# Performance work log

Hardware: AMD Instinct MI355X
Metric: run time of the kernel (lower is better)

## Reference

```python
import jax, jax.numpy as jnp
import numpy as np

EPS_ATTN = 1e-6
LN_EPS = 1e-5

def _layernorm(x, g, b):
    mu = jnp.mean(x, axis=-1, keepdims=True)
    var = jnp.var(x, axis=-1, keepdims=True)
    return (x - mu) * jax.lax.rsqrt(var + LN_EPS) * g + b

def _phi(x):
    return jax.nn.elu(x) + 1.0

def setup_inputs() -> dict:
    key = jax.random.key(0)
    ks = jax.random.split(key, 8)
    B, T, D, H = 2, 4096, 128, 128  # D = token_dim = d+1, H = hidden_dim
    s = 0.02
    return {
        "tokens": jax.random.normal(ks[0], (B, T, D), dtype=jnp.float32),
        "Wq": jax.random.normal(ks[1], (D, H), dtype=jnp.float32) * s,
        "Wk": jax.random.normal(ks[2], (D, H), dtype=jnp.float32) * s,
        "Wv": jax.random.normal(ks[3], (D, D), dtype=jnp.float32) * s,
        "Wg": jax.random.normal(ks[4], (D, D), dtype=jnp.float32) * s,
        "bg": jnp.zeros((D,), dtype=jnp.float32),
        "Wo": jax.random.normal(ks[5], (D, D), dtype=jnp.float32) * s,
        "g1": jnp.ones((D,), dtype=jnp.float32),
        "b1": jnp.zeros((D,), dtype=jnp.float32),
        "g2": jnp.ones((D,), dtype=jnp.float32),
        "b2": jnp.zeros((D,), dtype=jnp.float32),
    }

def reference(tokens, Wq, Wk, Wv, Wg, bg, Wo, g1, b1, g2, b2):
    x = _layernorm(tokens, g1, b1)                 # (b,t,m)
    Q = x @ Wq                                     # (b,t,h)
    K = x @ Wk                                     # (b,t,h)
    V = x @ Wv                                     # (b,t,m)
    G = jax.nn.sigmoid(x @ Wg + bg)                # (b,t,m)
    Vg = V * G
    Qp = _phi(Q)
    Kp = _phi(K)
    # causal linear attention via cumulative outer products
    kv = jnp.einsum('bth,btm->bthm', Kp, Vg)       # (b,t,h,m)
    S_kv = jnp.cumsum(kv, axis=1)
    S_k = jnp.cumsum(Kp, axis=1)
    numerator = jnp.einsum('bth,bthm->btm', Qp, S_kv)
    denom = jnp.maximum(jnp.einsum('bth,bth->bt', Qp, S_k), EPS_ATTN)
    attn_out = numerator / denom[..., None]
    out = tokens + (attn_out @ Wo) * 0.1
    return _layernorm(out, g2, b2)
```

## Files before the change

kernel.cpp:

```cpp
#include <hip/hip_runtime.h>
#include <math.h>

#define D_ 128
#define NTOK 8192
#define CHUNK 64
#define NCB 64
#define NCH 128
#define LN_EPS 1e-5f
#define EPS_ATTN 1e-6f

typedef __attribute__((ext_vector_type(8))) short bf16x8;
typedef __attribute__((ext_vector_type(4))) short bf16x4;
typedef __attribute__((ext_vector_type(2))) short bf16x2;
typedef __attribute__((ext_vector_type(4))) float f32x4;

__device__ inline short f2bf(float f) {
  unsigned u = __builtin_bit_cast(unsigned, f);
  u += 0x7fffu + ((u >> 16) & 1u);
  return (short)(u >> 16);
}
__device__ inline float bf2f(short s) {
  unsigned u = ((unsigned)(unsigned short)s) << 16;
  return __builtin_bit_cast(float, u);
}
__device__ inline float phi_(float x) { return x > 0.f ? x + 1.f : __expf(x); }

__global__ __launch_bounds__(256) void k_prep(const float* __restrict__ tokens,
    const float* __restrict__ Wq, const float* __restrict__ Wk,
    const float* __restrict__ Wv, const float* __restrict__ Wg,
    const float* __restrict__ Wo,
    const float* __restrict__ g1, const float* __restrict__ b1,
    short* __restrict__ WT, short* __restrict__ xln) {
  const int tid = threadIdx.x, bid = blockIdx.x;
  __shared__ float lds[64][132];
  if (bid < 10) {
    const int mat = bid >> 1, half = bid & 1;
    const float* W = mat==0?Wq: mat==1?Wk: mat==2?Wv: mat==3?Wg:Wo;
    short* o = WT + mat*D_*D_;
    #pragma unroll
    for (int it = 0; it < 8; ++it) {
      const int f = it*1024 + tid*4;
      const int kk = f >> 7, n = f & 127;
      const float4 v = *(const float4*)&W[(half*64 + kk)*D_ + n];
      lds[kk][n] = v.x; lds[kk][n+1] = v.y; lds[kk][n+2] = v.z; lds[kk][n+3] = v.w;
    }
    __syncthreads();
    #pragma unroll
    for (int it = 0; it < 8; ++it) {
      const int f = it*1024 + tid*4;
      const int n = f >> 6, kl = f & 63;
      bf16x4 ov;
      ov.x = f2bf(lds[kl][n]);   ov.y = f2bf(lds[kl+1][n]);
      ov.z = f2bf(lds[kl+2][n]); ov.w = f2bf(lds[kl+3][n]);
      *(bf16x4*)&o[n*D_ + half*64 + kl] = ov;
    }
    return;
  }
  const int m0 = (bid - 10) * 32;
  const int w = tid >> 6, l = tid & 63;
  const float2 gg = *(const float2*)&g1[l*2];
  const float2 bb = *(const float2*)&b1[l*2];
  float2 tv[8];
  #pragma unroll
  for (int it = 0; it < 8; ++it)
    tv[it] = *(const float2*)&tokens[(m0 + w*8 + it)*D_ + l*2];
  #pragma unroll
  for (int it = 0; it < 8; ++it) {
    const float2 v = tv[it];
    float s = v.x + v.y, qq = v.x*v.x + v.y*v.y;
    #pragma unroll
    for (int off = 1; off < 64; off <<= 1) {
      s += __shfl_xor(s, off); qq += __shfl_xor(qq, off);
    }
    const float mean = s*(1.f/D_);
    const float r2 = rsqrtf(qq*(1.f/D_) - mean*mean + LN_EPS);
    bf16x2 o;
    o.x = f2bf((v.x-mean)*r2*gg.x + bb.x);
    o.y = f2bf((v.y-mean)*r2*gg.y + bb.y);
    *(bf16x2*)&xln[(m0 + w*8 + it)*D_ + l*2] = o;
  }
}

__global__ __launch_bounds__(256) void k_qkvg(const short* __restrict__ xln,
    const short* __restrict__ WT, const float* __restrict__ bgp,
    short* __restrict__ Qp, short* __restrict__ Kp, short* __restrict__ KpT,
    short* __restrict__ VgT) {
  const int tid = threadIdx.x, bid = blockIdx.x;
  const int w = tid >> 6, l = tid & 63;
  const int i = l & 15, q = l >> 4;
  __shared__ short xs[32][136];
  __shared__ short wsd[128][136];

  auto stageW = [&](const short* __restrict__ Wb) {
    for (int v = tid; v < 2048; v += 256) {
      const int n = v >> 4, c8 = (v & 15)*8;
      *(bf16x8*)&wsd[n][c8] = *(const bf16x8*)&Wb[n*D_ + c8];
    }
  };
  auto stageX = [&](int m0) {
    for (int u = tid; u < 512; u += 256) {
      const int t = u >> 4, c8 = (u & 15)*8;
      *(bf16x8*)&xs[t][c8] = *(const bf16x8*)&xln[(m0 + t)*D_ + c8];
    }
  };
  auto gemm = [&](f32x4 (*acc)[2]) {
    #pragma unroll
    for (int kk = 0; kk < 4; ++kk) {
      bf16x8 a[2], bfr[2];
      #pragma unroll
      for (int mt = 0; mt < 2; ++mt) a[mt] = *(const bf16x8*)&xs[mt*16+i][kk*32+q*8];
      #pragma unroll
      for (int nt = 0; nt < 2; ++nt) bfr[nt] = *(const bf16x8*)&wsd[w*32+nt*16+i][kk*32+q*8];
      #pragma unroll
      for (int mt = 0; mt < 2; ++mt)
        #pragma unroll
        for (int nt = 0; nt < 2; ++nt)
          acc[mt][nt] = __builtin_amdgcn_mfma_f32_16x16x32_bf16(a[mt], bfr[nt], acc[mt][nt], 0, 0, 0);
    }
  };

  if (bid < 256) {
    const int m0 = bid * 32;
    stageX(m0);
    stageW(WT + 2*D_*D_);
    __syncthreads();
    f32x4 acc[2][2], accg[2][2];
    #pragma unroll
    for (int mt = 0; mt < 2; ++mt)
      #pragma unroll
      for (int nt = 0; nt < 2; ++nt) acc[mt][nt] = (f32x4){0.f,0.f,0.f,0.f};
    gemm(acc);
    __syncthreads();
    stageW(WT + 3*D_*D_);
    __syncthreads();
    #pragma unroll
    for (int mt = 0; mt < 2; ++mt)
      #pragma unroll
      for (int nt = 0; nt < 2; ++nt) accg[mt][nt] = (f32x4){0.f,0.f,0.f,0.f};
    gemm(accg);
    #pragma unroll
    for (int mt = 0; mt < 2; ++mt)
      #pragma unroll
      for (int nt = 0; nt < 2; ++nt) {
        const int h = w*32 + nt*16 + i;
        const int t0 = m0 + mt*16 + 4*q;
        const float bgd = bgp[h];
        bf16x4 o;
        #pragma unroll
        for (int r = 0; r < 4; ++r) {
          const float gv = 1.f/(1.f + __expf(-(accg[mt][nt][r] + bgd)));
          o[r] = f2bf(acc[mt][nt][r] * gv);
        }
        *(bf16x4*)&VgT[h*NTOK + t0] = o;
      }
  } else if (bid < 384) {
    stageW(WT);
    for (int uu = 0; uu < 2; ++uu) {
      const int m0 = ((bid - 256)*2 + uu) * 32;
      __syncthreads();
      stageX(m0);
      __syncthreads();
      f32x4 acc[2][2];
      #pragma unroll
      for (int mt = 0; mt < 2; ++mt)
        #pragma unroll
        for (int nt = 0; nt < 2; ++nt) acc[mt][nt] = (f32x4){0.f,0.f,0.f,0.f};
      gemm(acc);
      #pragma unroll
      for (int mt = 0; mt < 2; ++mt)
        #pragma unroll
        for (int nt = 0; nt < 2; ++nt) {
          const int h = w*32 + nt*16 + i;
          #pragma unroll
          for (int r = 0; r < 4; ++r)
            Qp[(m0 + mt*16 + 4*q + r)*D_ + h] = f2bf(phi_(acc[mt][nt][r]));
        }
    }
  } else {
    stageW(WT + D_*D_);
    for (int uu = 0; uu < 2; ++uu) {
      const int m0 = ((bid - 384)*2 + uu) * 32;
      __syncthreads();
      stageX(m0);
      __syncthreads();
      f32x4 acc[2][2];
      #pragma unroll
      for (int mt = 0; mt < 2; ++mt)
        #pragma unroll
        for (int nt = 0; nt < 2; ++nt) acc[mt][nt] = (f32x4){0.f,0.f,0.f,0.f};
      gemm(acc);
      #pragma unroll
      for (int mt = 0; mt < 2; ++mt)
        #pragma unroll
        for (int nt = 0; nt < 2; ++nt) {
          const int h = w*32 + nt*16 + i;
          const int t0 = m0 + mt*16 + 4*q;
          bf16x4 o;
          #pragma unroll
          for (int r = 0; r < 4; ++r) {
            const short bv = f2bf(phi_(acc[mt][nt][r]));
            Kp[(t0+r)*D_ + h] = bv;
            o[r] = bv;
          }
          *(bf16x4*)&KpT[h*NTOK + t0] = o;
        }
    }
  }
}

__global__ __launch_bounds__(256) void k_cs(const short* __restrict__ KpT,
    const short* __restrict__ VgT, const short* __restrict__ Qp,
    const short* __restrict__ Kp,
    float* __restrict__ KVT, float* __restrict__ Ksum,
    short* __restrict__ A, float* __restrict__ rowsum) {
  const int tid = threadIdx.x, bid = blockIdx.x;
  const int w = tid >> 6, l = tid & 63;
  const int i = l & 15, q = l >> 4;
  __shared__ __align__(16) char smem[34816];

  auto chunkkv = [&](int v) {
    const int c = v & 127, hh = (v >> 7) & 1, dh = v >> 8;
    const int tb = c*CHUNK;
    short (*vgl)[72] = (short(*)[72])smem;
    short (*kpl)[72] = (short(*)[72])(smem + 9216);
    float (*ksp)[5]  = (float(*)[5])(smem + 18432);
    for (int u = tid; u < 512; u += 256) {
      const int dd = u >> 3, c8 = (u & 7)*8;
      *(bf16x8*)&vgl[dd][c8] = *(const bf16x8*)&VgT[(dh*64+dd)*NTOK + tb + c8];
      *(bf16x8*)&kpl[dd][c8] = *(const bf16x8*)&KpT[(hh*64+dd)*NTOK + tb + c8];
    }
    __syncthreads();
    f32x4 acc[4];
    #pragma unroll
    for (int nt = 0; nt < 4; ++nt) acc[nt] = (f32x4){0.f,0.f,0.f,0.f};
    #pragma unroll
    for (int kk = 0; kk < 2; ++kk) {
      bf16x8 a = *(const bf16x8*)&vgl[w*16+i][kk*32+q*8];
      #pragma unroll
      for (int nt = 0; nt < 4; ++nt) {
        bf16x8 bb = *(const bf16x8*)&kpl[nt*16+i][kk*32+q*8];
        acc[nt] = __builtin_amdgcn_mfma_f32_16x16x32_bf16(a, bb, acc[nt], 0, 0, 0);
      }
    }
    float* KVc = KVT + (size_t)c*16384;
    #pragma unroll
    for (int nt = 0; nt < 4; ++nt)
      #pragma unroll
      for (int r = 0; r < 4; ++r) {
        const int d = dh*64 + w*16 + 4*q + r;
        const int h = hh*64 + nt*16 + i;
        KVc[d*D_ + h] = acc[nt][r];
      }
    if (dh == 0) {
      const int hq = tid >> 2, part = tid & 3;
      float s = 0.f;
      #pragma unroll
      for (int t = 0; t < 16; ++t) s += bf2f(kpl[hq][part*16 + t]);
      ksp[hq][part] = s;
      __syncthreads();
      if (tid < 64)
        Ksum[c*D_ + hh*64 + tid] = ksp[tid][0]+ksp[tid][1]+ksp[tid][2]+ksp[tid][3];
    }
  };

  auto scores = [&](int c) {
    const int tb = c*CHUNK;
    short (*qpl)[136] = (short(*)[136])smem;
    short (*kpl)[136] = (short(*)[136])(smem + 17408);
    for (int u = tid; u < 1024; u += 256) {
      const int t = u >> 4, c8 = (u & 15)*8;
      *(bf16x8*)&qpl[t][c8] = *(const bf16x8*)&Qp[(tb+t)*D_ + c8];
      *(bf16x8*)&kpl[t][c8] = *(const bf16x8*)&Kp[(tb+t)*D_ + c8];
    }
    __syncthreads();
    f32x4 acc[4];
    #pragma unroll
    for (int nt = 0; nt < 4; ++nt) acc[nt] = (f32x4){0.f,0.f,0.f,0.f};
    #pragma unroll
    for (int kk = 0; kk < 4; ++kk) {
      bf16x8 a = *(const bf16x8*)&qpl[w*16+i][kk*32+q*8];
      #pragma unroll
      for (int nt = 0; nt < 4; ++nt) {
        if (nt <= w) {
          bf16x8 bb = *(const bf16x8*)&kpl[nt*16+i][kk*32+q*8];
          acc[nt] = __builtin_amdgcn_mfma_f32_16x16x32_bf16(a, bb, acc[nt], 0, 0, 0);
        }
      }
    }
    short* Ac = A + c*4096;
    float rs[4] = {0.f,0.f,0.f,0.f};
    #pragma unroll
    for (int nt = 0; nt < 4; ++nt) {
      #pragma unroll
      for (int r = 0; r < 4; ++r) {
        const int t = w*16 + 4*q + r;
        const int s = nt*16 + i;
        const float v = (nt <= w && s <= t) ? acc[nt][r] : 0.f;
        rs[r] += v;
        Ac[t*64 + s] = f2bf(v);
      }
    }
    #pragma unroll
    for (int r = 0; r < 4; ++r) {
      #pragma unroll
      for (int off = 1; off < 16; off <<= 1) rs[r] += __shfl_xor(rs[r], off);
    }
    if (i == 0) {
      #pragma unroll
      for (int r = 0; r < 4; ++r) rowsum[c*64 + w*16 + 4*q + r] = rs[r];
    }
  };

  if (bid < 128) {
    scores(bid);
    __syncthreads();
    chunkkv(384 + bid);
  } else {
    chunkkv(bid - 128);
  }
}

__global__ __launch_bounds__(256) void k_scan(const float* __restrict__ KVT,
    short* __restrict__ KVTb, float* __restrict__ Ksum) {
  const int tid = threadIdx.x;
  if (blockIdx.x < 128) {
    const int b = blockIdx.x >> 6;
    const int e = (blockIdx.x & 63)*256 + tid;
    const size_t base = (size_t)b*NCB*16384 + e;
    float run = 0.f;
    #pragma unroll 8
    for (int c = 0; c < NCB; ++c) {
      const float v = KVT[base + (size_t)c*16384];
      KVTb[base + (size_t)c*16384] = f2bf(run);
      run += v;
    }
    return;
  }
  const int b = tid >> 7, h = tid & 127;
  float run = 0.f;
  #pragma unroll 8
  for (int c = 0; c < NCB; ++c) {
    const int idx = (b*NCB + c)*128 + h;
    const float v = Ksum[idx];
    Ksum[idx] = run;
    run += v;
  }
}

__global__ __launch_bounds__(256) void k_attnout(const short* __restrict__ Aintra,
    const short* __restrict__ Qp, const short* __restrict__ VgT,
    const short* __restrict__ KVTb, const float* __restrict__ Ksum,
    const float* __restrict__ rowsum, short* __restrict__ attn) {
  const int bid = blockIdx.x, tid = threadIdx.x;
  const int c = bid & 127, dq = bid >> 7;
  const int tb = c*CHUNK;
  __shared__ short at[64][200], bt[32][200];
  __shared__ float ksl[128], dpart[64][4], denl[64];
  const short* Ac = Aintra + c*4096;
  #pragma unroll
  for (int u = tid; u < 512; u += 256) {
    const int t = u >> 3, c8 = (u & 7)*8;
    *(bf16x8*)&at[t][c8] = *(const bf16x8*)&Ac[t*64 + c8];
  }
  #pragma unroll
  for (int u = tid; u < 1024; u += 256) {
    const int t = u >> 4, c8 = (u & 15)*8;
    *(bf16x8*)&at[t][64 + c8] = *(const bf16x8*)&Qp[(tb+t)*D_ + c8];
  }
  for (int u = tid; u < 256; u += 256) {
    const int dd = u >> 3, c8 = (u & 7)*8;
    *(bf16x8*)&bt[dd][c8] = *(const bf16x8*)&VgT[(dq*32+dd)*NTOK + tb + c8];
  }
  #pragma unroll
  for (int u = tid; u < 512; u += 256) {
    const int dd = u >> 4, c8 = (u & 15)*8;
    *(bf16x8*)&bt[dd][64 + c8] = *(const bf16x8*)&KVTb[(size_t)c*16384 + (dq*32+dd)*D_ + c8];
  }
  if (tid < 128) ksl[tid] = Ksum[c*128 + tid];
  __syncthreads();
  {
    const int t = tid >> 2, part = tid & 3;
    float dot = 0.f;
    #pragma unroll
    for (int h = 0; h < 32; ++h) dot += bf2f(at[t][64 + part*32 + h]) * ksl[part*32 + h];
    dpart[t][part] = dot;
  }
  __syncthreads();
  if (tid < 64)
    denl[tid] = fmaxf(rowsum[c*64 + tid] + dpart[tid][0]+dpart[tid][1]+dpart[tid][2]+dpart[tid][3], EPS_ATTN);
  __syncthreads();
  const int w = tid >> 6, l = tid & 63, i = l & 15, q = l >> 4;
  f32x4 acc[2];
  #pragma unroll
  for (int nt = 0; nt < 2; ++nt) acc[nt] = (f32x4){0.f,0.f,0.f,0.f};
  #pragma unroll
  for (int kk = 0; kk < 6; ++kk) {
    bf16x8 a = *(const bf16x8*)&at[w*16+i][kk*32+q*8];
    #pragma unroll
    for (int nt = 0; nt < 2; ++nt) {
      bf16x8 bb = *(const bf16x8*)&bt[nt*16+i][kk*32+q*8];
      acc[nt] = __builtin_amdgcn_mfma_f32_16x16x32_bf16(a, bb, acc[nt], 0, 0, 0);
    }
  }
  #pragma unroll
  for (int r = 0; r < 4; ++r) {
    const int t = w*16 + 4*q + r;
    const float inv = 1.f / denl[t];
    #pragma unroll
    for (int nt = 0; nt < 2; ++nt)
      attn[(size_t)(tb+t)*D_ + dq*32 + nt*16 + i] = f2bf(acc[nt][r] * inv);
  }
}

__global__ __launch_bounds__(256) void k_outln2(const short* __restrict__ attn,
    const short* __restrict__ WoT, const float* __restrict__ tokens,
    const float* __restrict__ g2, const float* __restrict__ b2,
    float* __restrict__ out) {
  const int m0 = blockIdx.x*32, tid = threadIdx.x;
  __shared__ short al[32][136], wl[128][136];
  __shared__ float tl[32][132];
  __shared__ float suml[32][4], ssql[32][4];
  __shared__ float meanl[32], rstdl[32];
  __shared__ float gl[128], bl2[128];
  for (int u = tid; u < 512; u += 256) {
    const int t = u >> 4, c8 = (u & 15)*8;
    *(bf16x8*)&al[t][c8] = *(const bf16x8*)&attn[(m0+t)*D_ + c8];
  }
  #pragma unroll
  for (int u = tid; u < 2048; u += 256) {
    const int n = u >> 4, c8 = (u & 15)*8;
    *(bf16x8*)&wl[n][c8] = *(const bf16x8*)&WoT[n*D_ + c8];
  }
  #pragma unroll
  for (int u = tid; u < 1024; u += 256) {
    const int t = u >> 5, c4 = (u & 31)*4;
    *(float4*)&tl[t][c4] = *(const float4*)&tokens[(m0+t)*D_ + c4];
  }
  if (tid < 128) { gl[tid] = g2[tid]; bl2[tid] = b2[tid]; }
  __syncthreads();
  const int w = tid >> 6, l = tid & 63, i = l & 15, q = l >> 4;
  f32x4 acc[2][2];
  #pragma unroll
  for (int mt = 0; mt < 2; ++mt)
    #pragma unroll
    for (int j = 0; j < 2; ++j) acc[mt][j] = (f32x4){0.f,0.f,0.f,0.f};
  #pragma unroll
  for (int kk = 0; kk < 4; ++kk) {
    bf16x8 a[2];
    #pragma unroll
    for (int mt = 0; mt < 2; ++mt) a[mt] = *(const bf16x8*)&al[mt*16+i][kk*32+q*8];
    #pragma unroll
    for (int j = 0; j < 2; ++j) {
      bf16x8 bb = *(const bf16x8*)&wl[(w*2+j)*16+i][kk*32+q*8];
      #pragma unroll
      for (int mt = 0; mt < 2; ++mt)
        acc[mt][j] = __builtin_amdgcn_mfma_f32_16x16x32_bf16(a[mt], bb, acc[mt][j], 0, 0, 0);
    }
  }
  float p[2][4][2];
  #pragma unroll
  for (int mt = 0; mt < 2; ++mt)
    #pragma unroll
    for (int r = 0; r < 4; ++r) {
      const int t = mt*16 + 4*q + r;
      float ps = 0.f, qs = 0.f;
      #pragma unroll
      for (int j = 0; j < 2; ++j) {
        const int col = w*32 + j*16 + i;
        const float v = tl[t][col] + 0.1f*acc[mt][j][r];
        p[mt][r][j] = v; ps += v; qs += v*v;
      }
      #pragma unroll
      for (int off = 1; off < 16; off <<= 1) {
        ps += __shfl_xor(ps, off); qs += __shfl_xor(qs, off);
      }
      if (i == 0) { suml[t][w] = ps; ssql[t][w] = qs; }
    }
  __syncthreads();
  if (tid < 32) {
    const float s = suml[tid][0]+suml[tid][1]+suml[tid][2]+suml[tid][3];
    const float qq = ssql[tid][0]+ssql[tid][1]+ssql[tid][2]+ssql[tid][3];
    const float mean = s*(1.f/D_);
    meanl[tid] = mean;
    rstdl[tid] = rsqrtf(qq*(1.f/D_) - mean*mean + LN_EPS);
  }
  __syncthreads();
  #pragma unroll
  for (int mt = 0; mt < 2; ++mt)
    #pragma unroll
    for (int r = 0; r < 4; ++r) {
      const int t = mt*16 + 4*q + r;
      const float mean = meanl[t], rr = rstdl[t];
      #pragma unroll
      for (int j = 0; j < 2; ++j) {
        const int col = w*32 + j*16 + i;
        out[(m0+t)*D_ + col] = (p[mt][r][j]-mean)*rr*gl[col] + bl2[col];
      }
    }
}

extern "C" void kernel_launch(void* const* d_in, const int* in_sizes, int n_in,
                              void* d_out, int out_size, void* d_ws, size_t ws_size,
                              hipStream_t stream) {
  const float* tokens = (const float*)d_in[0];
  const float* Wq = (const float*)d_in[1];
  const float* Wk = (const float*)d_in[2];
  const float* Wv = (const float*)d_in[3];
  const float* Wg = (const float*)d_in[4];
  const float* bg = (const float*)d_in[5];
  const float* Wo = (const float*)d_in[6];
  const float* g1 = (const float*)d_in[7];
  const float* b1 = (const float*)d_in[8];
  const float* g2 = (const float*)d_in[9];
  const float* b2 = (const float*)d_in[10];

  char* base = (char*)d_ws;
  short* Qp     = (short*)(base);
  short* Kp     = (short*)(base + (2u<<20));
  short* KpT    = (short*)(base + (4u<<20));
  short* VgT    = (short*)(base + (6u<<20));
  short* attn   = (short*)(base + (8u<<20));
  short* KVTb   = (short*)(base + (10u<<20));
  short* Aintra = (short*)(base + (14u<<20));
  short* WT     = (short*)(base + (15u<<20));
  float* rowsum = (float*)(base + (15u<<20) + (256u<<10));
  float* Ksum   = (float*)(base + (15u<<20) + (512u<<10));
  float* KVT    = (float*)(base + (16u<<20));
  short* xln    = (short*)(base + (24u<<20));

  short* WoT = WT + 4*D_*D_;

  k_prep<<<266, 256, 0, stream>>>(tokens, Wq, Wk, Wv, Wg, Wo, g1, b1, WT, xln);
  k_qkvg<<<512, 256, 0, stream>>>(xln, WT, bg, Qp, Kp, KpT, VgT);
  k_cs<<<512, 256, 0, stream>>>(KpT, VgT, Qp, Kp, KVT, Ksum, Aintra, rowsum);
  k_scan<<<129, 256, 0, stream>>>(KVT, KVTb, Ksum);
  k_attnout<<<512, 256, 0, stream>>>(Aintra, Qp, VgT, KVTb, Ksum, rowsum, attn);
  k_outln2<<<NTOK/32, 256, 0, stream>>>(attn, WoT, tokens, g2, b2, (float*)d_out);
}
```

Measured before the change: 112.6 us.

## Fuse LayerNorm and weight prep into QKVG, fuse attention output with Wo+LN2

Removes the separate prep kernel: each QKVG block now computes LayerNorm of its token rows directly into shared memory and transposes/converts the fp32 weights to bf16 while staging them. Attention output and the final Wo projection plus second LayerNorm are merged into one kernel. Each block handles 32 rows with all 128 output columns, and the normalized attention result stays in shared memory. This drops two launches and the xln/attn round trips through global memory. The cost is redundant weight conversion in every block, LayerNorm recomputed in Q and K blocks, and larger shared memory use with fewer blocks in the fused output kernel.

After: 112.8 us. No clear change (+0.1%).

```diff
diff --git a/kernel.cpp b/kernel.cpp
--- a/kernel.cpp
+++ b/kernel.cpp
@@ -25,64 +25,11 @@
 }
 __device__ inline float phi_(float x) { return x > 0.f ? x + 1.f : __expf(x); }
 
-__global__ __launch_bounds__(256) void k_prep(const float* __restrict__ tokens,
+__global__ __launch_bounds__(256) void k_qkvg(const float* __restrict__ tokens,
     const float* __restrict__ Wq, const float* __restrict__ Wk,
     const float* __restrict__ Wv, const float* __restrict__ Wg,
-    const float* __restrict__ Wo,
+    const float* __restrict__ bgp,
     const float* __restrict__ g1, const float* __restrict__ b1,
-    short* __restrict__ WT, short* __restrict__ xln) {
-  const int tid = threadIdx.x, bid = blockIdx.x;
-  __shared__ float lds[64][132];
-  if (bid < 10) {
-    const int mat = bid >> 1, half = bid & 1;
-    const float* W = mat==0?Wq: mat==1?Wk: mat==2?Wv: mat==3?Wg:Wo;
-    short* o = WT + mat*D_*D_;
-    #pragma unroll
-    for (int it = 0; it < 8; ++it) {
-      const int f = it*1024 + tid*4;
-      const int kk = f >> 7, n = f & 127;
-      const float4 v = *(const float4*)&W[(half*64 + kk)*D_ + n];
-      lds[kk][n] = v.x; lds[kk][n+1] = v.y; lds[kk][n+2] = v.z; lds[kk][n+3] = v.w;
-    }
-    __syncthreads();
-    #pragma unroll
-    for (int it = 0; it < 8; ++it) {
-      const int f = it*1024 + tid*4;
-      const int n = f >> 6, kl = f & 63;
-      bf16x4 ov;
-      ov.x = f2bf(lds[kl][n]);   ov.y = f2bf(lds[kl+1][n]);
-      ov.z = f2bf(lds[kl+2][n]); ov.w = f2bf(lds[kl+3][n]);
-      *(bf16x4*)&o[n*D_ + half*64 + kl] = ov;
-    }
-    return;
-  }
-  const int m0 = (bid - 10) * 32;
-  const int w = tid >> 6, l = tid & 63;
-  const float2 gg = *(const float2*)&g1[l*2];
-  const float2 bb = *(const float2*)&b1[l*2];
-  float2 tv[8];
-  #pragma unroll
-  for (int it = 0; it < 8; ++it)
-    tv[it] = *(const float2*)&tokens[(m0 + w*8 + it)*D_ + l*2];
-  #pragma unroll
-  for (int it = 0; it < 8; ++it) {
-    const float2 v = tv[it];
-    float s = v.x + v.y, qq = v.x*v.x + v.y*v.y;
-    #pragma unroll
-    for (int off = 1; off < 64; off <<= 1) {
-      s += __shfl_xor(s, off); qq += __shfl_xor(qq, off);
-    }
-    const float mean = s*(1.f/D_);
-    const float r2 = rsqrtf(qq*(1.f/D_) - mean*mean + LN_EPS);
-    bf16x2 o;
-    o.x = f2bf((v.x-mean)*r2*gg.x + bb.x);
-    o.y = f2bf((v.y-mean)*r2*gg.y + bb.y);
-    *(bf16x2*)&xln[(m0 + w*8 + it)*D_ + l*2] = o;
-  }
-}
-
-__global__ __launch_bounds__(256) void k_qkvg(const short* __restrict__ xln,
-    const short* __restrict__ WT, const float* __restrict__ bgp,
     short* __restrict__ Qp, short* __restrict__ Kp, short* __restrict__ KpT,
     short* __restrict__ VgT) {
   const int tid = threadIdx.x, bid = blockIdx.x;
@@ -91,16 +38,39 @@
   __shared__ short xs[32][136];
   __shared__ short wsd[128][136];
 
-  auto stageW = [&](const short* __restrict__ Wb) {
-    for (int v = tid; v < 2048; v += 256) {
-      const int n = v >> 4, c8 = (v & 15)*8;
-      *(bf16x8*)&wsd[n][c8] = *(const bf16x8*)&Wb[n*D_ + c8];
+  auto stageWT = [&](const float* __restrict__ Wf) {
+    #pragma unroll
+    for (int it = 0; it < 16; ++it) {
+      const int v = it*256 + tid;
+      const int k = v & 127, n4 = v >> 7;
+      const float4 x4 = *(const float4*)&Wf[k*D_ + n4*4];
+      wsd[n4*4+0][k] = f2bf(x4.x);
+      wsd[n4*4+1][k] = f2bf(x4.y);
+      wsd[n4*4+2][k] = f2bf(x4.z);
+      wsd[n4*4+3][k] = f2bf(x4.w);
     }
   };
-  auto stageX = [&](int m0) {
-    for (int u = tid; u < 512; u += 256) {
-      const int t = u >> 4, c8 = (u & 15)*8;
-      *(bf16x8*)&xs[t][c8] = *(const bf16x8*)&xln[(m0 + t)*D_ + c8];
+  auto doLN = [&](int m0) {
+    const float2 gg = *(const float2*)&g1[l*2];
+    const float2 bb = *(const float2*)&b1[l*2];
+    float2 tv[8];
+    #pragma unroll
+    for (int it = 0; it < 8; ++it)
+      tv[it] = *(const float2*)&tokens[(m0 + w*8 + it)*D_ + l*2];
+    #pragma unroll
+    for (int it = 0; it < 8; ++it) {
+      const float2 v = tv[it];
+      float s = v.x + v.y, qq = v.x*v.x + v.y*v.y;
+      #pragma unroll
+      for (int off = 1; off < 64; off <<= 1) {
+        s += __shfl_xor(s, off); qq += __shfl_xor(qq, off);
+      }
+      const float mean = s*(1.f/D_);
+      const float r2 = rsqrtf(qq*(1.f/D_) - mean*mean + LN_EPS);
+      bf16x2 o;
+      o.x = f2bf((v.x-mean)*r2*gg.x + bb.x);
+      o.y = f2bf((v.y-mean)*r2*gg.y + bb.y);
+      *(bf16x2*)&xs[w*8 + it][l*2] = o;
     }
   };
   auto gemm = [&](f32x4 (*acc)[2]) {
@@ -121,8 +91,8 @@
 
   if (bid < 256) {
     const int m0 = bid * 32;
-    stageX(m0);
-    stageW(WT + 2*D_*D_);
+    doLN(m0);
+    stageWT(Wv);
     __syncthreads();
     f32x4 acc[2][2], accg[2][2];
     #pragma unroll
@@ -131,7 +101,7 @@
       for (int nt = 0; nt < 2; ++nt) acc[mt][nt] = (f32x4){0.f,0.f,0.f,0.f};
     gemm(acc);
     __syncthreads();
-    stageW(WT + 3*D_*D_);
+    stageWT(Wg);
     __syncthreads();
     #pragma unroll
     for (int mt = 0; mt < 2; ++mt)
@@ -154,11 +124,11 @@
         *(bf16x4*)&VgT[h*NTOK + t0] = o;
       }
   } else if (bid < 384) {
-    stageW(WT);
+    stageWT(Wq);
     for (int uu = 0; uu < 2; ++uu) {
       const int m0 = ((bid - 256)*2 + uu) * 32;
       __syncthreads();
-      stageX(m0);
+      doLN(m0);
       __syncthreads();
       f32x4 acc[2][2];
       #pragma unroll
@@ -177,11 +147,11 @@
         }
     }
   } else {
-    stageW(WT + D_*D_);
+    stageWT(Wk);
     for (int uu = 0; uu < 2; ++uu) {
       const int m0 = ((bid - 384)*2 + uu) * 32;
       __syncthreads();
-      stageX(m0);
+      doLN(m0);
       __syncthreads();
       f32x4 acc[2][2];
       #pragma unroll
@@ -347,156 +317,141 @@
   }
 }
 
-__global__ __launch_bounds__(256) void k_attnout(const short* __restrict__ Aintra,
+__global__ __launch_bounds__(256) void k_ao2(const short* __restrict__ Aintra,
     const short* __restrict__ Qp, const short* __restrict__ VgT,
     const short* __restrict__ KVTb, const float* __restrict__ Ksum,
-    const float* __restrict__ rowsum, short* __restrict__ attn) {
+    const float* __restrict__ rowsum, const float* __restrict__ Wo,
+    const float* __restrict__ tokens, const float* __restrict__ g2,
+    const float* __restrict__ b2, float* __restrict__ out) {
   const int bid = blockIdx.x, tid = threadIdx.x;
-  const int c = bid & 127, dq = bid >> 7;
-  const int tb = c*CHUNK;
-  __shared__ short at[64][200], bt[32][200];
-  __shared__ float ksl[128], dpart[64][4], denl[64];
+  const int c = bid >> 1, half = bid & 1;
+  const int tb = c*CHUNK, t0 = tb + half*32;
+  __shared__ __align__(16) char smem[73856];
+  short (*at)[200] = (short(*)[200])smem;
+  short (*bt)[200] = (short(*)[200])(smem + 12800);
+  float* ksl        = (float*)(smem + 64000);
+  float (*dpart)[4] = (float(*)[4])(smem + 64512);
+  float* denl       = (float*)(smem + 65024);
+  short (*al)[136]  = (short(*)[136])(smem + 65152);
+  short (*wl)[136]  = (short(*)[136])smem;
+  float (*tl)[132]  = (float(*)[132])(smem + 34816);
+  float* gl         = (float*)(smem + 51712);
+  float* bl2        = (float*)(smem + 52224);
+  float (*suml)[2]  = (float(*)[2])(smem + 52736);
+  float (*ssql)[2]  = (float(*)[2])(smem + 52992);
+
   const short* Ac = Aintra + c*4096;
-  #pragma unroll
+  for (int u = tid; u < 256; u += 256) {
+    const int tr = u >> 3, c8 = (u & 7)*8;
+    *(bf16x8*)&at[tr][c8] = *(const bf16x8*)&Ac[(half*32+tr)*64 + c8];
+  }
   for (int u = tid; u < 512; u += 256) {
-    const int t = u >> 3, c8 = (u & 7)*8;
-    *(bf16x8*)&at[t][c8] = *(const bf16x8*)&Ac[t*64 + c8];
-  }
-  #pragma unroll
+    const int tr = u >> 4, c8 = (u & 15)*8;
+    *(bf16x8*)&at[tr][64 + c8] = *(const bf16x8*)&Qp[(t0+tr)*D_ + c8];
+  }
   for (int u = tid; u < 1024; u += 256) {
-    const int t = u >> 4, c8 = (u & 15)*8;
-    *(bf16x8*)&at[t][64 + c8] = *(const bf16x8*)&Qp[(tb+t)*D_ + c8];
-  }
-  for (int u = tid; u < 256; u += 256) {
     const int dd = u >> 3, c8 = (u & 7)*8;
-    *(bf16x8*)&bt[dd][c8] = *(const bf16x8*)&VgT[(dq*32+dd)*NTOK + tb + c8];
-  }
-  #pragma unroll
-  for (int u = tid; u < 512; u += 256) {
+    *(bf16x8*)&bt[dd][c8] = *(const bf16x8*)&VgT[dd*NTOK + tb + c8];
+  }
+  for (int u = tid; u < 2048; u += 256) {
     const int dd = u >> 4, c8 = (u & 15)*8;
-    *(bf16x8*)&bt[dd][64 + c8] = *(const bf16x8*)&KVTb[(size_t)c*16384 + (dq*32+dd)*D_ + c8];
+    *(bf16x8*)&bt[dd][64 + c8] = *(const bf16x8*)&KVTb[(size_t)c*16384 + dd*D_ + c8];
   }
   if (tid < 128) ksl[tid] = Ksum[c*128 + tid];
   __syncthreads();
-  {
-    const int t = tid >> 2, part = tid & 3;
+  if (tid < 128) {
+    const int tr = tid >> 2, part = tid & 3;
     float dot = 0.f;
     #pragma unroll
-    for (int h = 0; h < 32; ++h) dot += bf2f(at[t][64 + part*32 + h]) * ksl[part*32 + h];
-    dpart[t][part] = dot;
-  }
-  __syncthreads();
-  if (tid < 64)
-    denl[tid] = fmaxf(rowsum[c*64 + tid] + dpart[tid][0]+dpart[tid][1]+dpart[tid][2]+dpart[tid][3], EPS_ATTN);
+    for (int h = 0; h < 32; ++h) dot += bf2f(at[tr][64 + part*32 + h]) * ksl[part*32 + h];
+    dpart[tr][part] = dot;
+  }
+  __syncthreads();
+  if (tid < 32)
+    denl[tid] = fmaxf(rowsum[c*64 + half*32 + tid] + dpart[tid][0]+dpart[tid][1]+dpart[tid][2]+dpart[tid][3], EPS_ATTN);
   __syncthreads();
   const int w = tid >> 6, l = tid & 63, i = l & 15, q = l >> 4;
-  f32x4 acc[2];
-  #pragma unroll
-  for (int nt = 0; nt < 2; ++nt) acc[nt] = (f32x4){0.f,0.f,0.f,0.f};
+  const int rt = w & 1, dh = w >> 1;
+  f32x4 acc[4];
+  #pragma unroll
+  for (int nt = 0; nt < 4; ++nt) acc[nt] = (f32x4){0.f,0.f,0.f,0.f};
   #pragma unroll
   for (int kk = 0; kk < 6; ++kk) {
-    bf16x8 a = *(const bf16x8*)&at[w*16+i][kk*32+q*8];
-    #pragma unroll
-    for (int nt = 0; nt < 2; ++nt) {
-      bf16x8 bb = *(const bf16x8*)&bt[nt*16+i][kk*32+q*8];
+    bf16x8 a = *(const bf16x8*)&at[rt*16+i][kk*32+q*8];
+    #pragma unroll
+    for (int nt = 0; nt < 4; ++nt) {
+      bf16x8 bb = *(const bf16x8*)&bt[dh*64+nt*16+i][kk*32+q*8];
       acc[nt] = __builtin_amdgcn_mfma_f32_16x16x32_bf16(a, bb, acc[nt], 0, 0, 0);
     }
   }
   #pragma unroll
   for (int r = 0; r < 4; ++r) {
-    const int t = w*16 + 4*q + r;
+    const int t = rt*16 + 4*q + r;
     const float inv = 1.f / denl[t];
     #pragma unroll
-    for (int nt = 0; nt < 2; ++nt)
-      attn[(size_t)(tb+t)*D_ + dq*32 + nt*16 + i] = f2bf(acc[nt][r] * inv);
-  }
-}
-
-__global__ __launch_bounds__(256) void k_outln2(const short* __restrict__ attn,
-    const short* __restrict__ WoT, const float* __restrict__ tokens,
-    const float* __restrict__ g2, const float* __restrict__ b2,
-    float* __restrict__ out) {
-  const int m0 = blockIdx.x*32, tid = threadIdx.x;
-  __shared__ short al[32][136], wl[128][136];
-  __shared__ float tl[32][132];
-  __shared__ float suml[32][4], ssql[32][4];
-  __shared__ float meanl[32], rstdl[32];
-  __shared__ float gl[128], bl2[128];
-  for (int u = tid; u < 512; u += 256) {
-    const int t = u >> 4, c8 = (u & 15)*8;
-    *(bf16x8*)&al[t][c8] = *(const bf16x8*)&attn[(m0+t)*D_ + c8];
-  }
-  #pragma unroll
-  for (int u = tid; u < 2048; u += 256) {
-    const int n = u >> 4, c8 = (u & 15)*8;
-    *(bf16x8*)&wl[n][c8] = *(const bf16x8*)&WoT[n*D_ + c8];
-  }
-  #pragma unroll
+    for (int nt = 0; nt < 4; ++nt)
+      al[t][dh*64 + nt*16 + i] = f2bf(acc[nt][r] * inv);
+  }
+  __syncthreads();
+  #pragma unroll
+  for (int it = 0; it < 16; ++it) {
+    const int v = it*256 + tid;
+    const int k = v & 127, n4 = v >> 7;
+    const float4 x4 = *(const float4*)&Wo[k*D_ + n4*4];
+    wl[n4*4+0][k] = f2bf(x4.x);
+    wl[n4*4+1][k] = f2bf(x4.y);
+    wl[n4*4+2][k] = f2bf(x4.z);
+    wl[n4*4+3][k] = f2bf(x4.w);
+  }
   for (int u = tid; u < 1024; u += 256) {
-    const int t = u >> 5, c4 = (u & 31)*4;
-    *(float4*)&tl[t][c4] = *(const float4*)&tokens[(m0+t)*D_ + c4];
+    const int tr = u >> 5, c4 = (u & 31)*4;
+    *(float4*)&tl[tr][c4] = *(const float4*)&tokens[(t0+tr)*D_ + c4];
   }
   if (tid < 128) { gl[tid] = g2[tid]; bl2[tid] = b2[tid]; }
   __syncthreads();
-  const int w = tid >> 6, l = tid & 63, i = l & 15, q = l >> 4;
-  f32x4 acc[2][2];
-  #pragma unroll
-  for (int mt = 0; mt < 2; ++mt)
-    #pragma unroll
-    for (int j = 0; j < 2; ++j) acc[mt][j] = (f32x4){0.f,0.f,0.f,0.f};
+  f32x4 acc2[4];
+  #pragma unroll
+  for (int nt = 0; nt < 4; ++nt) acc2[nt] = (f32x4){0.f,0.f,0.f,0.f};
   #pragma unroll
   for (int kk = 0; kk < 4; ++kk) {
-    bf16x8 a[2];
-    #pragma unroll
-    for (int mt = 0; mt < 2; ++mt) a[mt] = *(const bf16x8*)&al[mt*16+i][kk*32+q*8];
-    #pragma unroll
-    for (int j = 0; j < 2; ++j) {
-      bf16x8 bb = *(const bf16x8*)&wl[(w*2+j)*16+i][kk*32+q*8];
-      #pragma unroll
-      for (int mt = 0; mt < 2; ++mt)
-        acc[mt][j] = __builtin_amdgcn_mfma_f32_16x16x32_bf16(a[mt], bb, acc[mt][j], 0, 0, 0);
-    }
-  }
-  float p[2][4][2];
-  #pragma unroll
-  for (int mt = 0; mt < 2; ++mt)
-    #pragma unroll
-    for (int r = 0; r < 4; ++r) {
-      const int t = mt*16 + 4*q + r;
-      float ps = 0.f, qs = 0.f;
-      #pragma unroll
-      for (int j = 0; j < 2; ++j) {
-        const int col = w*32 + j*16 + i;
-        const float v = tl[t][col] + 0.1f*acc[mt][j][r];
-        p[mt][r][j] = v; ps += v; qs += v*v;
-      }
-      #pragma unroll
-      for (int off = 1; off < 16; off <<= 1) {
-        ps += __shfl_xor(ps, off); qs += __shfl_xor(qs, off);
-      }
-      if (i == 0) { suml[t][w] = ps; ssql[t][w] = qs; }
-    }
-  __syncthreads();
-  if (tid < 32) {
-    const float s = suml[tid][0]+suml[tid][1]+suml[tid][2]+suml[tid][3];
-    const float qq = ssql[tid][0]+ssql[tid][1]+ssql[tid][2]+ssql[tid][3];
+    bf16x8 a = *(const bf16x8*)&al[rt*16+i][kk*32+q*8];
+    #pragma unroll
+    for (int nt = 0; nt < 4; ++nt) {
+      bf16x8 bb = *(const bf16x8*)&wl[dh*64+nt*16+i][kk*32+q*8];
+      acc2[nt] = __builtin_amdgcn_mfma_f32_16x16x32_bf16(a, bb, acc2[nt], 0, 0, 0);
+    }
+  }
+  float p[4][4];
+  #pragma unroll
+  for (int r = 0; r < 4; ++r) {
+    const int t = rt*16 + 4*q + r;
+    float ps = 0.f, qs = 0.f;
+    #pragma unroll
+    for (int nt = 0; nt < 4; ++nt) {
+      const int col = dh*64 + nt*16 + i;
+      const float v = tl[t][col] + 0.1f*acc2[nt][r];
+      p[r][nt] = v; ps += v; qs += v*v;
+    }
+    #pragma unroll
+    for (int off = 1; off < 16; off <<= 1) {
+      ps += __shfl_xor(ps, off); qs += __shfl_xor(qs, off);
+    }
+    if (i == 0) { suml[t][dh] = ps; ssql[t][dh] = qs; }
+  }
+  __syncthreads();
+  #pragma unroll
+  for (int r = 0; r < 4; ++r) {
+    const int t = rt*16 + 4*q + r;
+    const float s = suml[t][0] + suml[t][1];
+    const float qq = ssql[t][0] + ssql[t][1];
     const float mean = s*(1.f/D_);
-    meanl[tid] = mean;
-    rstdl[tid] = rsqrtf(qq*(1.f/D_) - mean*mean + LN_EPS);
-  }
-  __syncthreads();
-  #pragma unroll
-  for (int mt = 0; mt < 2; ++mt)
-    #pragma unroll
-    for (int r = 0; r < 4; ++r) {
-      const int t = mt*16 + 4*q + r;
-      const float mean = meanl[t], rr = rstdl[t];
-      #pragma unroll
-      for (int j = 0; j < 2; ++j) {
-        const int col = w*32 + j*16 + i;
-        out[(m0+t)*D_ + col] = (p[mt][r][j]-mean)*rr*gl[col] + bl2[col];
-      }
-    }
+    const float rr = rsqrtf(qq*(1.f/D_) - mean*mean + LN_EPS);
+    #pragma unroll
+    for (int nt = 0; nt < 4; ++nt) {
+      const int col = dh*64 + nt*16 + i;
+      out[(size_t)(t0+t)*D_ + col] = (p[r][nt]-mean)*rr*gl[col] + bl2[col];
+    }
+  }
 }
 
 extern "C" void kernel_launch(void* const* d_in, const int* in_sizes, int n_in,
@@ -519,21 +474,16 @@
   short* Kp     = (short*)(base + (2u<<20));
   short* KpT    = (short*)(base + (4u<<20));
   short* VgT    = (short*)(base + (6u<<20));
-  short* attn   = (short*)(base + (8u<<20));
-  short* KVTb   = (short*)(base + (10u<<20));
-  short* Aintra = (short*)(base + (14u<<20));
-  short* WT     = (short*)(base + (15u<<20));
-  float* rowsum = (float*)(base + (15u<<20) + (256u<<10));
-  float* Ksum   = (float*)(base + (15u<<20) + (512u<<10));
+  short* KVTb   = (short*)(base + (8u<<20));
+  short* Aintra = (short*)(base + (12u<<20));
+  float* rowsum = (float*)(base + (13u<<20));
+  float* Ksum   = (float*)(base + (13u<<20) + (256u<<10));
   float* KVT    = (float*)(base + (16u<<20));
-  short* xln    = (short*)(base + (24u<<20));
-
-  short* WoT = WT + 4*D_*D_;
-
-  k_prep<<<266, 256, 0, stream>>>(tokens, Wq, Wk, Wv, Wg, Wo, g1, b1, WT, xln);
-  k_qkvg<<<512, 256, 0, stream>>>(xln, WT, bg, Qp, Kp, KpT, VgT);
+
+  k_qkvg<<<512, 256, 0, stream>>>(tokens, Wq, Wk, Wv, Wg, bg, g1, b1,
+                                  Qp, Kp, KpT, VgT);
   k_cs<<<512, 256, 0, stream>>>(KpT, VgT, Qp, Kp, KVT, Ksum, Aintra, rowsum);
   k_scan<<<129, 256, 0, stream>>>(KVT, KVTb, Ksum);
-  k_attnout<<<512, 256, 0, stream>>>(Aintra, Qp, VgT, KVTb, Ksum, rowsum, attn);
-  k_outln2<<<NTOK/32, 256, 0, stream>>>(attn, WoT, tokens, g2, b2, (float*)d_out);
-}
+  k_ao2<<<256, 256, 0, stream>>>(Aintra, Qp, VgT, KVTb, Ksum, rowsum, Wo,
+                                 tokens, g2, b2, (float*)d_out);
+}
```
